# Performance work log

Measured on AMD Instinct MI355X. Metric: run time of the kernel, lower is better.

Reference implementation:

```python
import jax, jax.numpy as jnp
import numpy as np

B, C, S, W, H = 4, 512, 1, 64, 64
D = C // 8  # query/key channel dim from Conv2d(in_dim, in_dim // 8, 1)
N = W * H


def setup_inputs() -> dict:
    key = jax.random.key(0)
    ks = jax.random.split(key, 8)
    s_in = 1.0 / np.sqrt(C)
    return {
        "x": jax.random.normal(ks[0], (B, C, S, W, H), dtype=jnp.float32),
        "Wq": jax.random.normal(ks[1], (D, C), dtype=jnp.float32) * s_in,
        "bq": jax.random.normal(ks[2], (D,), dtype=jnp.float32) * 0.01,
        "Wk": jax.random.normal(ks[3], (D, C), dtype=jnp.float32) * s_in,
        "bk": jax.random.normal(ks[4], (D,), dtype=jnp.float32) * 0.01,
        "Wv": jax.random.normal(ks[5], (C, C), dtype=jnp.float32) * s_in,
        "bv": jax.random.normal(ks[6], (C,), dtype=jnp.float32) * 0.01,
        "gamma": jax.random.uniform(ks[7], (1,), dtype=jnp.float32),
        "crop_h": 64,
        "crop_w": 64,
    }


def reference(x, Wq, bq, Wk, bk, Wv, bv, gamma, crop_h, crop_w):
    # x: [B, C, 1, W, H] -> flatten spatial to tokens: [B, C, N]
    b, c, s, w, h = x.shape
    n = w * h
    xs = x[:, :, 0].reshape(b, c, n)
    # 1x1 convs == channel matmuls
    q = jnp.einsum('dc,bcn->bnd', Wq, xs) + bq  # [B, N, D] (proj_query, permuted)
    k = jnp.einsum('dc,bcn->bdn', Wk, xs) + bk[:, None]  # [B, D, N]
    energy = jnp.einsum('bnd,bdm->bnm', q, k)  # [B, N, N]
    attention = jax.nn.softmax(energy, axis=-1)  # softmax over last dim
    v = jnp.einsum('dc,bcn->bdn', Wv, xs) + bv[:, None]  # [B, C, N]
    # out = bmm(value, attention^T): [B, C, N]
    out = jnp.einsum('bcn,bmn->bcm', v, attention)
    out = out.reshape(b, c, w, h)
    out = gamma[0] * out + x[:, :, 0]
    return out, attention
```

## Files before the change

kernel.cpp:

```cpp
#include <hip/hip_runtime.h>
#include <hip/hip_bf16.h>


#define B_ 4
#define C_ 512
#define D_ 64
#define N_ 4096

typedef __hip_bfloat16 bf16;
typedef __attribute__((ext_vector_type(8))) short bf16x8;
typedef __attribute__((ext_vector_type(4))) float f32x4;

__device__ __forceinline__ void gload16(const void* g, void* l) {
    __builtin_amdgcn_global_load_lds(
        (__attribute__((address_space(1))) void*)g,
        (__attribute__((address_space(3))) void*)l, 16, 0, 0);
}

__global__ __launch_bounds__(256) void prep_weights(
        const float* __restrict__ Wq, const float* __restrict__ Wk,
        const float* __restrict__ Wv,
        float* __restrict__ WqT, float* __restrict__ WkT,
        bf16* __restrict__ Wvb) {
    int i = blockIdx.x * 256 + threadIdx.x;
    if (i < 32768) {
        int d = i >> 9, c = i & 511;
        WqT[c * 64 + d] = Wq[i];
    } else if (i < 65536) {
        int j = i - 32768;
        int d = j >> 9, c = j & 511;
        WkT[c * 64 + d] = Wk[j];
    } else {
        int j = i - 65536;
        if (j < 262144) Wvb[j] = __float2bfloat16(Wv[j]);
    }
}

__global__ __launch_bounds__(256) void transpose_cast(const float* __restrict__ x,
                                                      bf16* __restrict__ xT) {
    __shared__ bf16 tile[32][33];
    int b = blockIdx.z;
    int n0 = blockIdx.x * 32;
    int c0 = blockIdx.y * 32;
    int tx = threadIdx.x;
    int ty = threadIdx.y;
    const float* xb = x + (size_t)b * C_ * N_;
    bf16* xTb = xT + (size_t)b * N_ * C_;
#pragma unroll
    for (int k = 0; k < 32; k += 8)
        tile[ty + k][tx] = __float2bfloat16(xb[(size_t)(c0 + ty + k) * N_ + n0 + tx]);
    __syncthreads();
#pragma unroll
    for (int k = 0; k < 32; k += 8)
        xTb[(size_t)(n0 + ty + k) * C_ + c0 + tx] = tile[tx][ty + k];
}

__global__ __launch_bounds__(256) void proj_qk(
        const float* __restrict__ x,
        const float* __restrict__ WqT, const float* __restrict__ WkT,
        const float* __restrict__ bq, const float* __restrict__ bk,
        bf16* __restrict__ Qh, bf16* __restrict__ Ql,
        bf16* __restrict__ Kh, bf16* __restrict__ Kl) {
    int b = blockIdx.y;
    int z = blockIdx.z;
    int which = z >> 2;
    int dh = (z & 3) * 16;
    int n = blockIdx.x * 256 + threadIdx.x;
    const float* WT = which ? WkT : WqT;
    const float* bias = which ? bk : bq;
    bf16* Hd = (which ? Kh : Qh) + ((size_t)b * N_ + n) * 64 + dh;
    bf16* Ld = (which ? Kl : Ql) + ((size_t)b * N_ + n) * 64 + dh;
    const float* xb = x + (size_t)b * C_ * N_;

    float acc[16];
#pragma unroll
    for (int d = 0; d < 16; d++) acc[d] = 0.f;

    for (int c = 0; c < 512; c++) {
        float xv = xb[(size_t)c * N_ + n];
        const float* wrow = WT + c * 64 + dh;
#pragma unroll
        for (int d = 0; d < 16; d += 4) {
            float4 w = *(const float4*)(wrow + d);
            acc[d + 0] += w.x * xv;
            acc[d + 1] += w.y * xv;
            acc[d + 2] += w.z * xv;
            acc[d + 3] += w.w * xv;
        }
    }

    bf16x8 h0, h1, l0, l1;
    bf16* hp0 = (bf16*)&h0;
    bf16* hp1 = (bf16*)&h1;
    bf16* lp0 = (bf16*)&l0;
    bf16* lp1 = (bf16*)&l1;
#pragma unroll
    for (int d = 0; d < 8; d++) {
        float v = acc[d] + bias[dh + d];
        bf16 h = __float2bfloat16(v);
        hp0[d] = h;
        lp0[d] = __float2bfloat16(v - __bfloat162float(h));
    }
#pragma unroll
    for (int d = 8; d < 16; d++) {
        float v = acc[d] + bias[dh + d];
        bf16 h = __float2bfloat16(v);
        hp1[d - 8] = h;
        lp1[d - 8] = __float2bfloat16(v - __bfloat162float(h));
    }
    *(bf16x8*)(Hd)     = h0;
    *(bf16x8*)(Hd + 8) = h1;
    *(bf16x8*)(Ld)     = l0;
    *(bf16x8*)(Ld + 8) = l1;
}

__global__ __launch_bounds__(256, 2) void proj_v(
        const bf16* __restrict__ Wvb, const bf16* __restrict__ xTb,
        const float* __restrict__ bv, bf16* __restrict__ V) {
    int b = blockIdx.z;
    int r0 = blockIdx.y * 128;
    int n0 = blockIdx.x * 128;
    int tid = threadIdx.x;
    int wv = tid >> 6;
    int lane = tid & 63;
    int l15 = lane & 15;
    int kq  = lane >> 4;
    int wr = wv >> 1;
    int wc = wv & 1;

    __shared__ bf16 Ws[128 * 32];
    __shared__ bf16 Xs[128 * 32];

    const bf16* Bb = xTb + (size_t)b * N_ * C_;

    int srow = tid >> 2;
    int scol = (tid & 3) * 8;
    bf16* WsW0 = Ws + wv * 512;
    bf16* XsW0 = Xs + wv * 512;

    f32x4 acc[4][4];
#pragma unroll
    for (int i = 0; i < 4; i++)
#pragma unroll
        for (int j = 0; j < 4; j++)
#pragma unroll
            for (int r = 0; r < 4; r++) acc[i][j][r] = 0.f;

    for (int kt = 0; kt < C_; kt += 32) {
#pragma unroll
        for (int rnd = 0; rnd < 2; rnd++) {
            int row = srow + rnd * 64;
            gload16(Wvb + (size_t)(r0 + row) * C_ + kt + scol, WsW0 + rnd * 2048);
            gload16(Bb + (size_t)(n0 + row) * C_ + kt + scol, XsW0 + rnd * 2048);
        }
        __syncthreads();

        bf16x8 af[4], bfr[4];
#pragma unroll
        for (int i = 0; i < 4; i++)
            af[i] = *(const bf16x8*)(Ws + (wr * 64 + i * 16 + l15) * 32 + kq * 8);
#pragma unroll
        for (int j = 0; j < 4; j++)
            bfr[j] = *(const bf16x8*)(Xs + (wc * 64 + j * 16 + l15) * 32 + kq * 8);
#pragma unroll
        for (int i = 0; i < 4; i++)
#pragma unroll
            for (int j = 0; j < 4; j++)
                acc[i][j] = __builtin_amdgcn_mfma_f32_16x16x32_bf16(af[i], bfr[j], acc[i][j], 0, 0, 0);
        __syncthreads();
    }

    bf16* Vb = V + (size_t)b * C_ * N_;
#pragma unroll
    for (int i = 0; i < 4; i++)
#pragma unroll
        for (int r = 0; r < 4; r++) {
            int row = r0 + wr * 64 + i * 16 + kq * 4 + r;
            float bvv = bv[row];
#pragma unroll
            for (int j = 0; j < 4; j++) {
                int col = n0 + wc * 64 + j * 16 + l15;
                Vb[(size_t)row * N_ + col] = __float2bfloat16(acc[i][j][r] + bvv);
            }
        }
}

__global__ __launch_bounds__(256, 4) void attn_fused(
        const bf16* __restrict__ Qh, const bf16* __restrict__ Ql,
        const bf16* __restrict__ Kh, const bf16* __restrict__ Kl,
        float* __restrict__ attF, bf16* __restrict__ attB) {
    int b = blockIdx.y;
    int n0 = blockIdx.x * 16;
    int tid = threadIdx.x;
    int wv = tid >> 6;
    int lane = tid & 63;
    int l15 = lane & 15;
    int kq = lane >> 4;

    const bf16* qhb = Qh + (size_t)b * N_ * 64;
    const bf16* qlb = Ql + (size_t)b * N_ * 64;
    const bf16* khb = Kh + (size_t)b * N_ * 64;
    const bf16* klb = Kl + (size_t)b * N_ * 64;

    const bf16* qrh = qhb + (size_t)(n0 + l15) * 64 + kq * 8;
    const bf16* qrl = qlb + (size_t)(n0 + l15) * 64 + kq * 8;
    bf16x8 bh0 = *(const bf16x8*)(qrh);
    bf16x8 bh1 = *(const bf16x8*)(qrh + 32);
    bf16x8 bl0 = *(const bf16x8*)(qrl);
    bf16x8 bl1 = *(const bf16x8*)(qrl + 32);

    const bf16* kwh = khb + (size_t)(wv * 1024 + l15) * 64 + kq * 8;
    const bf16* kwl = klb + (size_t)(wv * 1024 + l15) * 64 + kq * 8;

    float m = -3.0e38f, sl = 0.f;

    for (int j = 0; j < 64; j++) {
        const bf16* ph = kwh + (size_t)j * 1024;
        const bf16* pl = kwl + (size_t)j * 1024;
        bf16x8 a0 = *(const bf16x8*)(ph);
        bf16x8 a1 = *(const bf16x8*)(ph + 32);
        bf16x8 a2 = *(const bf16x8*)(pl);
        bf16x8 a3 = *(const bf16x8*)(pl + 32);
        f32x4 acc = {0.f, 0.f, 0.f, 0.f};
        acc = __builtin_amdgcn_mfma_f32_16x16x32_bf16(a0, bh0, acc, 0, 0, 0);
        acc = __builtin_amdgcn_mfma_f32_16x16x32_bf16(a1, bh1, acc, 0, 0, 0);
        acc = __builtin_amdgcn_mfma_f32_16x16x32_bf16(a0, bl0, acc, 0, 0, 0);
        acc = __builtin_amdgcn_mfma_f32_16x16x32_bf16(a1, bl1, acc, 0, 0, 0);
        acc = __builtin_amdgcn_mfma_f32_16x16x32_bf16(a2, bh0, acc, 0, 0, 0);
        acc = __builtin_amdgcn_mfma_f32_16x16x32_bf16(a3, bh1, acc, 0, 0, 0);
        float tm = fmaxf(fmaxf(acc[0], acc[1]), fmaxf(acc[2], acc[3]));
        float mn = fmaxf(m, tm);
        sl = sl * __expf(m - mn)
           + __expf(acc[0] - mn) + __expf(acc[1] - mn)
           + __expf(acc[2] - mn) + __expf(acc[3] - mn);
        m = mn;
    }

#pragma unroll
    for (int mask = 16; mask <= 32; mask <<= 1) {
        float om = __shfl_xor(m, mask, 64);
        float os = __shfl_xor(sl, mask, 64);
        float mn = fmaxf(m, om);
        sl = sl * __expf(m - mn) + os * __expf(om - mn);
        m = mn;
    }

    __shared__ float redM[16][4];
    __shared__ float redS[16][4];
    if (lane < 16) { redM[l15][wv] = m; redS[l15][wv] = sl; }
    __syncthreads();
    float m0r = redM[l15][0], m1r = redM[l15][1];
    float m2r = redM[l15][2], m3r = redM[l15][3];
    float mf = fmaxf(fmaxf(m0r, m1r), fmaxf(m2r, m3r));
    float sf = redS[l15][0] * __expf(m0r - mf) + redS[l15][1] * __expf(m1r - mf)
             + redS[l15][2] * __expf(m2r - mf) + redS[l15][3] * __expf(m3r - mf);
    float inv = 1.f / sf;

    float* af = attF + (size_t)b * N_ * N_ + (size_t)(n0 + l15) * N_
              + wv * 1024 + kq * 4;
    bf16* ab = attB ? attB + (size_t)b * N_ * N_ + (size_t)(n0 + l15) * N_
                       + wv * 1024 + kq * 4
                    : (bf16*)0;
    for (int j = 0; j < 64; j++) {
        const bf16* ph = kwh + (size_t)j * 1024;
        const bf16* pl = kwl + (size_t)j * 1024;
        bf16x8 a0 = *(const bf16x8*)(ph);
        bf16x8 a1 = *(const bf16x8*)(ph + 32);
        bf16x8 a2 = *(const bf16x8*)(pl);
        bf16x8 a3 = *(const bf16x8*)(pl + 32);
        f32x4 acc = {0.f, 0.f, 0.f, 0.f};
        acc = __builtin_amdgcn_mfma_f32_16x16x32_bf16(a0, bh0, acc, 0, 0, 0);
        acc = __builtin_amdgcn_mfma_f32_16x16x32_bf16(a1, bh1, acc, 0, 0, 0);
        acc = __builtin_amdgcn_mfma_f32_16x16x32_bf16(a0, bl0, acc, 0, 0, 0);
        acc = __builtin_amdgcn_mfma_f32_16x16x32_bf16(a1, bl1, acc, 0, 0, 0);
        acc = __builtin_amdgcn_mfma_f32_16x16x32_bf16(a2, bh0, acc, 0, 0, 0);
        acc = __builtin_amdgcn_mfma_f32_16x16x32_bf16(a3, bh1, acc, 0, 0, 0);
        float4 p;
        p.x = __expf(acc[0] - mf) * inv;
        p.y = __expf(acc[1] - mf) * inv;
        p.z = __expf(acc[2] - mf) * inv;
        p.w = __expf(acc[3] - mf) * inv;
        *(float4*)(af + j * 16) = p;
        if (ab) {
            bf16 pb[4] = {__float2bfloat16(p.x), __float2bfloat16(p.y),
                          __float2bfloat16(p.z), __float2bfloat16(p.w)};
            *(short4*)(ab + j * 16) = *(short4*)pb;
        }
    }
}

__global__ __launch_bounds__(256, 2) void pv_out_fast(
        const bf16* __restrict__ V, const bf16* __restrict__ attB,
        const float* __restrict__ x, const float* __restrict__ gamma,
        float* __restrict__ out) {
    int b = blockIdx.z;
    int c0 = blockIdx.y * 128;
    int m0 = blockIdx.x * 128;
    int tid = threadIdx.x;
    int wv = tid >> 6;
    int lane = tid & 63;
    int l15 = lane & 15;
    int kq  = lane >> 4;
    int wr = wv >> 1;
    int wc = wv & 1;

    __shared__ bf16 Vs[128 * 32];
    __shared__ bf16 As[128 * 32];

    const bf16* Vb = V + (size_t)b * C_ * N_;
    const bf16* Ab = attB + (size_t)b * N_ * N_;

    int srow = tid >> 2;
    int scol = (tid & 3) * 8;
    bf16* VsW0 = Vs + wv * 512;
    bf16* AsW0 = As + wv * 512;

    f32x4 acc[4][4];
#pragma unroll
    for (int i = 0; i < 4; i++)
#pragma unroll
        for (int j = 0; j < 4; j++)
#pragma unroll
            for (int r = 0; r < 4; r++) acc[i][j][r] = 0.f;

    for (int kt = 0; kt < N_; kt += 32) {
#pragma unroll
        for (int rnd = 0; rnd < 2; rnd++) {
            int row = srow + rnd * 64;
            gload16(Vb + (size_t)(c0 + row) * N_ + kt + scol, VsW0 + rnd * 2048);
            gload16(Ab + (size_t)(m0 + row) * N_ + kt + scol, AsW0 + rnd * 2048);
        }
        __syncthreads();

        bf16x8 af[4], bfr[4];
#pragma unroll
        for (int i = 0; i < 4; i++)
            af[i] = *(const bf16x8*)(Vs + (wr * 64 + i * 16 + l15) * 32 + kq * 8);
#pragma unroll
        for (int j = 0; j < 4; j++)
            bfr[j] = *(const bf16x8*)(As + (wc * 64 + j * 16 + l15) * 32 + kq * 8);
#pragma unroll
        for (int i = 0; i < 4; i++)
#pragma unroll
            for (int j = 0; j < 4; j++)
                acc[i][j] = __builtin_amdgcn_mfma_f32_16x16x32_bf16(af[i], bfr[j], acc[i][j], 0, 0, 0);
        __syncthreads();
    }

    float g = gamma[0];
    const float* xb = x + (size_t)b * C_ * N_;
    float* ob = out + (size_t)b * C_ * N_;
#pragma unroll
    for (int i = 0; i < 4; i++)
#pragma unroll
        for (int j = 0; j < 4; j++)
#pragma unroll
            for (int r = 0; r < 4; r++) {
                int row = c0 + wr * 64 + i * 16 + kq * 4 + r;
                int col = m0 + wc * 64 + j * 16 + l15;
                size_t idx = (size_t)row * N_ + col;
                ob[idx] = g * acc[i][j][r] + xb[idx];
            }
}

__global__ __launch_bounds__(256, 2) void pv_out(
        const bf16* __restrict__ V, const bf16* __restrict__ attB,
        const float* __restrict__ attF,
        const float* __restrict__ x, const float* __restrict__ gamma,
        float* __restrict__ out) {
    int b = blockIdx.z;
    int wave = threadIdx.x >> 6;
    int c0 = blockIdx.y * 128 + (wave >> 1) * 64;
    int m0 = blockIdx.x * 128 + (wave & 1) * 64;
    int lane = threadIdx.x & 63;
    int l15 = lane & 15;
    int kq  = lane >> 4;

    const bf16* Vb = V + (size_t)b * C_ * N_;
    const bf16* AbB = attB ? attB + (size_t)b * N_ * N_ : (const bf16*)0;
    const float* AbF = attF + (size_t)b * N_ * N_;

    f32x4 acc[4][4];
#pragma unroll
    for (int i = 0; i < 4; i++)
#pragma unroll
        for (int j = 0; j < 4; j++)
#pragma unroll
            for (int r = 0; r < 4; r++) acc[i][j][r] = 0.f;

    for (int n = 0; n < N_; n += 32) {
        bf16x8 af[4], bfr[4];
#pragma unroll
        for (int i = 0; i < 4; i++)
            af[i] = *(const bf16x8*)(Vb + (size_t)(c0 + i * 16 + l15) * N_ + n + kq * 8);
        if (AbB) {
#pragma unroll
            for (int j = 0; j < 4; j++)
                bfr[j] = *(const bf16x8*)(AbB + (size_t)(m0 + j * 16 + l15) * N_ + n + kq * 8);
        } else {
#pragma unroll
            for (int j = 0; j < 4; j++) {
                const float* ap = AbF + (size_t)(m0 + j * 16 + l15) * N_ + n + kq * 8;
                float4 u = *(const float4*)ap;
                float4 w = *(const float4*)(ap + 4);
                bf16x8 bb;
                bf16* pb = (bf16*)&bb;
                pb[0] = __float2bfloat16(u.x); pb[1] = __float2bfloat16(u.y);
                pb[2] = __float2bfloat16(u.z); pb[3] = __float2bfloat16(u.w);
                pb[4] = __float2bfloat16(w.x); pb[5] = __float2bfloat16(w.y);
                pb[6] = __float2bfloat16(w.z); pb[7] = __float2bfloat16(w.w);
                bfr[j] = bb;
            }
        }
#pragma unroll
        for (int i = 0; i < 4; i++)
#pragma unroll
            for (int j = 0; j < 4; j++)
                acc[i][j] = __builtin_amdgcn_mfma_f32_16x16x32_bf16(af[i], bfr[j], acc[i][j], 0, 0, 0);
    }

    float g = gamma[0];
    const float* xb = x + (size_t)b * C_ * N_;
    float* ob = out + (size_t)b * C_ * N_;
#pragma unroll
    for (int i = 0; i < 4; i++)
#pragma unroll
        for (int j = 0; j < 4; j++)
#pragma unroll
            for (int r = 0; r < 4; r++) {
                int row = c0 + i * 16 + kq * 4 + r;
                int col = m0 + j * 16 + l15;
                size_t idx = (size_t)row * N_ + col;
                ob[idx] = g * acc[i][j][r] + xb[idx];
            }
}

extern "C" void kernel_launch(void* const* d_in, const int* in_sizes, int n_in,
                              void* d_out, int out_size, void* d_ws, size_t ws_size,
                              hipStream_t stream) {
    const float* x     = (const float*)d_in[0];
    const float* Wq    = (const float*)d_in[1];
    const float* bq    = (const float*)d_in[2];
    const float* Wk    = (const float*)d_in[3];
    const float* bk    = (const float*)d_in[4];
    const float* Wv    = (const float*)d_in[5];
    const float* bv    = (const float*)d_in[6];
    const float* gamma = (const float*)d_in[7];
    (void)in_sizes; (void)n_in; (void)out_size;

    float* out  = (float*)d_out;
    float* attF = out + (size_t)B_ * C_ * N_;

    char* ws = (char*)d_ws;
    bf16*  qh  = (bf16*) (ws + 0);
    bf16*  ql  = (bf16*) (ws + 2097152);
    bf16*  kh  = (bf16*) (ws + 4194304);
    bf16*  kl  = (bf16*) (ws + 6291456);
    bf16*  V   = (bf16*) (ws + 8388608);
    bf16*  xTb = (bf16*) (ws + 25165824);
    float* WqT = (float*)(ws + 41943040);
    float* WkT = (float*)(ws + 42074112);
    bf16*  Wvb = (bf16*) (ws + 42205184);
    bf16*  attB = (bf16*)(ws + 42729472);
    const size_t full_need = 42729472ULL + (size_t)B_ * N_ * N_ * 2;
    bf16* attB_use = (ws_size >= full_need) ? attB : (bf16*)0;

    prep_weights<<<1280, 256, 0, stream>>>(Wq, Wk, Wv, WqT, WkT, Wvb);

    transpose_cast<<<dim3(N_ / 32, C_ / 32, B_), dim3(32, 8), 0, stream>>>(x, xTb);

    proj_qk<<<dim3(N_ / 256, B_, 8), 256, 0, stream>>>(x, WqT, WkT, bq, bk,
                                                       qh, ql, kh, kl);

    proj_v<<<dim3(N_ / 128, C_ / 128, B_), 256, 0, stream>>>(Wvb, xTb, bv, V);

    attn_fused<<<dim3(N_ / 16, B_), 256, 0, stream>>>(qh, ql, kh, kl,
                                                      attF, attB_use);

    if (attB_use) {
        pv_out_fast<<<dim3(N_ / 128, C_ / 128, B_), 256, 0, stream>>>(
            V, attB_use, x, gamma, out);
    } else {
        pv_out<<<dim3(N_ / 128, C_ / 128, B_), 256, 0, stream>>>(
            V, attB_use, attF, x, gamma, out);
    }
}
```

Before: 842.1 us.

## Stage K tiles in swizzled LDS and double query rows per attention block

The attention kernel now handles 32 query rows per block instead of 16, with waves split 2x2 over query rows and key halves. K hi/lo tiles of 64 keys are loaded cooperatively into LDS with global_load_lds, using an XOR swizzle to avoid bank conflicts. Each K tile is then shared across query rows rather than each wave reading K from global memory on its own. This cuts global/L2 traffic for K but adds two barriers per tile and gives no double buffering, so the loads are not overlapped with compute.

```diff
diff --git a/kernel.cpp b/kernel.cpp
--- a/kernel.cpp
+++ b/kernel.cpp
@@ -190,49 +190,86 @@
         const bf16* __restrict__ Kh, const bf16* __restrict__ Kl,
         float* __restrict__ attF, bf16* __restrict__ attB) {
     int b = blockIdx.y;
-    int n0 = blockIdx.x * 16;
+    int n0 = blockIdx.x * 32;
     int tid = threadIdx.x;
     int wv = tid >> 6;
+    int wr = wv >> 1;
+    int wc = wv & 1;
     int lane = tid & 63;
     int l15 = lane & 15;
     int kq = lane >> 4;
 
+    __shared__ bf16 Ks[2][2][64 * 64];
+    __shared__ float redM[32][2];
+    __shared__ float redS[32][2];
+
     const bf16* qhb = Qh + (size_t)b * N_ * 64;
     const bf16* qlb = Ql + (size_t)b * N_ * 64;
-    const bf16* khb = Kh + (size_t)b * N_ * 64;
-    const bf16* klb = Kl + (size_t)b * N_ * 64;
-
-    const bf16* qrh = qhb + (size_t)(n0 + l15) * 64 + kq * 8;
-    const bf16* qrl = qlb + (size_t)(n0 + l15) * 64 + kq * 8;
+    const bf16* khl = (wr ? Kl : Kh) + (size_t)b * N_ * 64;
+
+    int qrow = n0 + wr * 16 + l15;
+    const bf16* qrh = qhb + (size_t)qrow * 64 + kq * 8;
+    const bf16* qrl = qlb + (size_t)qrow * 64 + kq * 8;
     bf16x8 bh0 = *(const bf16x8*)(qrh);
     bf16x8 bh1 = *(const bf16x8*)(qrh + 32);
     bf16x8 bl0 = *(const bf16x8*)(qrl);
     bf16x8 bl1 = *(const bf16x8*)(qrl + 32);
-
-    const bf16* kwh = khb + (size_t)(wv * 1024 + l15) * 64 + kq * 8;
-    const bf16* kwl = klb + (size_t)(wv * 1024 + l15) * 64 + kq * 8;
+    asm volatile("" : "+v"(bh0), "+v"(bh1), "+v"(bl0), "+v"(bl1));
+
+    int srow_ = lane >> 3;
+    int schunk = (lane & 7) ^ srow_;
+    const bf16* ksrc = khl + (size_t)srow_ * 64 + schunk * 8;
+    bf16* kdst = &Ks[wc][wr][0];
+
+    int tr_base = l15;
+    int sw0 = ((kq) ^ (l15 & 7)) * 8;
+    int sw1 = ((4 + kq) ^ (l15 & 7)) * 8;
+
+    const bf16* khs = &Ks[wc][0][0];
+    const bf16* kls = &Ks[wc][1][0];
 
     float m = -3.0e38f, sl = 0.f;
 
-    for (int j = 0; j < 64; j++) {
-        const bf16* ph = kwh + (size_t)j * 1024;
-        const bf16* pl = kwl + (size_t)j * 1024;
-        bf16x8 a0 = *(const bf16x8*)(ph);
-        bf16x8 a1 = *(const bf16x8*)(ph + 32);
-        bf16x8 a2 = *(const bf16x8*)(pl);
-        bf16x8 a3 = *(const bf16x8*)(pl + 32);
-        f32x4 acc = {0.f, 0.f, 0.f, 0.f};
-        acc = __builtin_amdgcn_mfma_f32_16x16x32_bf16(a0, bh0, acc, 0, 0, 0);
-        acc = __builtin_amdgcn_mfma_f32_16x16x32_bf16(a1, bh1, acc, 0, 0, 0);
-        acc = __builtin_amdgcn_mfma_f32_16x16x32_bf16(a0, bl0, acc, 0, 0, 0);
-        acc = __builtin_amdgcn_mfma_f32_16x16x32_bf16(a1, bl1, acc, 0, 0, 0);
-        acc = __builtin_amdgcn_mfma_f32_16x16x32_bf16(a2, bh0, acc, 0, 0, 0);
-        acc = __builtin_amdgcn_mfma_f32_16x16x32_bf16(a3, bh1, acc, 0, 0, 0);
-        float tm = fmaxf(fmaxf(acc[0], acc[1]), fmaxf(acc[2], acc[3]));
+    for (int t = 0; t < 32; t++) {
+        int t0 = wc * 2048 + t * 64;
+#pragma unroll
+        for (int r = 0; r < 8; r++)
+            gload16(ksrc + (size_t)(t0 + r * 8) * 64, kdst + r * 512);
+        __syncthreads();
+
+        f32x4 acc[4];
+#pragma unroll
+        for (int s = 0; s < 4; s++) {
+            int tr = s * 16 + tr_base;
+            const bf16* ph = khs + tr * 64;
+            const bf16* pl = kls + tr * 64;
+            bf16x8 a0 = *(const bf16x8*)(ph + sw0);
+            bf16x8 a1 = *(const bf16x8*)(ph + sw1);
+            bf16x8 a2 = *(const bf16x8*)(pl + sw0);
+            bf16x8 a3 = *(const bf16x8*)(pl + sw1);
+            f32x4 ac = {0.f, 0.f, 0.f, 0.f};
+            ac = __builtin_amdgcn_mfma_f32_16x16x32_bf16(a0, bh0, ac, 0, 0, 0);
+            ac = __builtin_amdgcn_mfma_f32_16x16x32_bf16(a1, bh1, ac, 0, 0, 0);
+            ac = __builtin_amdgcn_mfma_f32_16x16x32_bf16(a0, bl0, ac, 0, 0, 0);
+            ac = __builtin_amdgcn_mfma_f32_16x16x32_bf16(a1, bl1, ac, 0, 0, 0);
+            ac = __builtin_amdgcn_mfma_f32_16x16x32_bf16(a2, bh0, ac, 0, 0, 0);
+            ac = __builtin_amdgcn_mfma_f32_16x16x32_bf16(a3, bh1, ac, 0, 0, 0);
+            acc[s] = ac;
+        }
+        __syncthreads();
+
+        float tm = acc[0][0];
+#pragma unroll
+        for (int s = 0; s < 4; s++)
+#pragma unroll
+            for (int r = 0; r < 4; r++) tm = fmaxf(tm, acc[s][r]);
         float mn = fmaxf(m, tm);
-        sl = sl * __expf(m - mn)
-           + __expf(acc[0] - mn) + __expf(acc[1] - mn)
-           + __expf(acc[2] - mn) + __expf(acc[3] - mn);
+        float ssum = 0.f;
+#pragma unroll
+        for (int s = 0; s < 4; s++)
+#pragma unroll
+            for (int r = 0; r < 4; r++) ssum += __expf(acc[s][r] - mn);
+        sl = sl * __expf(m - mn) + ssum;
         m = mn;
     }
 
@@ -245,47 +282,55 @@
         m = mn;
     }
 
-    __shared__ float redM[16][4];
-    __shared__ float redS[16][4];
-    if (lane < 16) { redM[l15][wv] = m; redS[l15][wv] = sl; }
+    int row_local = wr * 16 + l15;
+    if (lane < 16) { redM[row_local][wc] = m; redS[row_local][wc] = sl; }
     __syncthreads();
-    float m0r = redM[l15][0], m1r = redM[l15][1];
-    float m2r = redM[l15][2], m3r = redM[l15][3];
-    float mf = fmaxf(fmaxf(m0r, m1r), fmaxf(m2r, m3r));
-    float sf = redS[l15][0] * __expf(m0r - mf) + redS[l15][1] * __expf(m1r - mf)
-             + redS[l15][2] * __expf(m2r - mf) + redS[l15][3] * __expf(m3r - mf);
+    float m0r = redM[row_local][0], m1r = redM[row_local][1];
+    float mf = fmaxf(m0r, m1r);
+    float sf = redS[row_local][0] * __expf(m0r - mf)
+             + redS[row_local][1] * __expf(m1r - mf);
     float inv = 1.f / sf;
 
-    float* af = attF + (size_t)b * N_ * N_ + (size_t)(n0 + l15) * N_
-              + wv * 1024 + kq * 4;
-    bf16* ab = attB ? attB + (size_t)b * N_ * N_ + (size_t)(n0 + l15) * N_
-                       + wv * 1024 + kq * 4
+    float* af = attF + (size_t)b * N_ * N_ + (size_t)qrow * N_ + wc * 2048 + kq * 4;
+    bf16* ab = attB ? attB + (size_t)b * N_ * N_ + (size_t)qrow * N_ + wc * 2048 + kq * 4
                     : (bf16*)0;
-    for (int j = 0; j < 64; j++) {
-        const bf16* ph = kwh + (size_t)j * 1024;
-        const bf16* pl = kwl + (size_t)j * 1024;
-        bf16x8 a0 = *(const bf16x8*)(ph);
-        bf16x8 a1 = *(const bf16x8*)(ph + 32);
-        bf16x8 a2 = *(const bf16x8*)(pl);
-        bf16x8 a3 = *(const bf16x8*)(pl + 32);
-        f32x4 acc = {0.f, 0.f, 0.f, 0.f};
-        acc = __builtin_amdgcn_mfma_f32_16x16x32_bf16(a0, bh0, acc, 0, 0, 0);
-        acc = __builtin_amdgcn_mfma_f32_16x16x32_bf16(a1, bh1, acc, 0, 0, 0);
-        acc = __builtin_amdgcn_mfma_f32_16x16x32_bf16(a0, bl0, acc, 0, 0, 0);
-        acc = __builtin_amdgcn_mfma_f32_16x16x32_bf16(a1, bl1, acc, 0, 0, 0);
-        acc = __builtin_amdgcn_mfma_f32_16x16x32_bf16(a2, bh0, acc, 0, 0, 0);
-        acc = __builtin_amdgcn_mfma_f32_16x16x32_bf16(a3, bh1, acc, 0, 0, 0);
-        float4 p;
-        p.x = __expf(acc[0] - mf) * inv;
-        p.y = __expf(acc[1] - mf) * inv;
-        p.z = __expf(acc[2] - mf) * inv;
-        p.w = __expf(acc[3] - mf) * inv;
-        *(float4*)(af + j * 16) = p;
-        if (ab) {
-            bf16 pb[4] = {__float2bfloat16(p.x), __float2bfloat16(p.y),
-                          __float2bfloat16(p.z), __float2bfloat16(p.w)};
-            *(short4*)(ab + j * 16) = *(short4*)pb;
-        }
+    for (int t = 0; t < 32; t++) {
+        int t0 = wc * 2048 + t * 64;
+#pragma unroll
+        for (int r = 0; r < 8; r++)
+            gload16(ksrc + (size_t)(t0 + r * 8) * 64, kdst + r * 512);
+        __syncthreads();
+
+#pragma unroll
+        for (int s = 0; s < 4; s++) {
+            int tr = s * 16 + tr_base;
+            const bf16* ph = khs + tr * 64;
+            const bf16* pl = kls + tr * 64;
+            bf16x8 a0 = *(const bf16x8*)(ph + sw0);
+            bf16x8 a1 = *(const bf16x8*)(ph + sw1);
+            bf16x8 a2 = *(const bf16x8*)(pl + sw0);
+            bf16x8 a3 = *(const bf16x8*)(pl + sw1);
+            f32x4 ac = {0.f, 0.f, 0.f, 0.f};
+            ac = __builtin_amdgcn_mfma_f32_16x16x32_bf16(a0, bh0, ac, 0, 0, 0);
+            ac = __builtin_amdgcn_mfma_f32_16x16x32_bf16(a1, bh1, ac, 0, 0, 0);
+            ac = __builtin_amdgcn_mfma_f32_16x16x32_bf16(a0, bl0, ac, 0, 0, 0);
+            ac = __builtin_amdgcn_mfma_f32_16x16x32_bf16(a1, bl1, ac, 0, 0, 0);
+            ac = __builtin_amdgcn_mfma_f32_16x16x32_bf16(a2, bh0, ac, 0, 0, 0);
+            ac = __builtin_amdgcn_mfma_f32_16x16x32_bf16(a3, bh1, ac, 0, 0, 0);
+            float4 p;
+            p.x = __expf(ac[0] - mf) * inv;
+            p.y = __expf(ac[1] - mf) * inv;
+            p.z = __expf(ac[2] - mf) * inv;
+            p.w = __expf(ac[3] - mf) * inv;
+            int coff = t * 64 + s * 16;
+            *(float4*)(af + coff) = p;
+            if (ab) {
+                bf16 pb[4] = {__float2bfloat16(p.x), __float2bfloat16(p.y),
+                              __float2bfloat16(p.z), __float2bfloat16(p.w)};
+                *(short4*)(ab + coff) = *(short4*)pb;
+            }
+        }
+        __syncthreads();
     }
 }
 
@@ -474,7 +519,7 @@
 
     proj_v<<<dim3(N_ / 128, C_ / 128, B_), 256, 0, stream>>>(Wvb, xTb, bv, V);
 
-    attn_fused<<<dim3(N_ / 16, B_), 256, 0, stream>>>(qh, ql, kh, kl,
+    attn_fused<<<dim3(N_ / 32, B_), 256, 0, stream>>>(qh, ql, kh, kl,
                                                       attF, attB_use);
 
     if (attB_use) {
```

Measured after the change: 699.1 us. -17.0%, faster.
